# Kernel tuning notes

Hardware: AMD Instinct MI355X
Metric: run time of the kernel (lower is better)

The kernel has to match this reference:

```python
import jax, jax.numpy as jnp
import numpy as np

N_HEADS = 16
D_EMB = 1024
D_HEAD = D_EMB // N_HEADS


def setup_inputs() -> dict:
    key = jax.random.key(0)
    ks = jax.random.split(key, 5)
    scale = 1.0 / np.sqrt(D_EMB)
    x = jax.random.normal(ks[0], (4, 2048, D_EMB), dtype=jnp.float32)
    W_in = jax.random.normal(ks[1], (3 * D_EMB, D_EMB), dtype=jnp.float32) * scale
    b_in = jax.random.normal(ks[2], (3 * D_EMB,), dtype=jnp.float32) * 0.01
    W_out = jax.random.normal(ks[3], (D_EMB, D_EMB), dtype=jnp.float32) * scale
    b_out = jax.random.normal(ks[4], (D_EMB,), dtype=jnp.float32) * 0.01
    return {"x": x, "W_in": W_in, "b_in": b_in, "W_out": W_out, "b_out": b_out}


def reference(x, W_in, b_in, W_out, b_out):
    b, s, d = x.shape
    qkv = x @ W_in.T + b_in  # [b, s, 3d]
    q, k, v = jnp.split(qkv, 3, axis=-1)
    def heads(t):
        return t.reshape(b, s, N_HEADS, D_HEAD).transpose(0, 2, 1, 3)  # [b,h,s,dh]
    q, k, v = heads(q), heads(k), heads(v)
    scores = jnp.einsum('bhqd,bhkd->bhqk', q, k)
    causal = jnp.tril(jnp.ones((s, s), dtype=bool))  # keep lower-triangular incl diag
    scores = jnp.where(causal, scores, -jnp.inf)
    scores = scores / np.sqrt(D_HEAD).astype(np.float32)
    w = jax.nn.softmax(scores, axis=-1)
    out = jnp.einsum('bhqk,bhkd->bhqd', w, v)  # [b,h,s,dh]
    out = out.transpose(0, 2, 1, 3).reshape(b, s, d)
    return out @ W_out.T + b_out
```

## Files before the change

### kernel.cpp

```cpp
#include <hip/hip_runtime.h>
#include <hip/hip_bf16.h>
#include <cstdint>


typedef float  floatx4  __attribute__((ext_vector_type(4)));
typedef __bf16 bf16x8   __attribute__((ext_vector_type(8)));
typedef __bf16 bf16x4   __attribute__((ext_vector_type(4)));
typedef short  shortx4  __attribute__((ext_vector_type(4)));
typedef unsigned int   uint32x2 __attribute__((ext_vector_type(2)));
typedef unsigned short ushortx8 __attribute__((ext_vector_type(8)));

#define MFMA16(a,b,c) __builtin_amdgcn_mfma_f32_16x16x32_bf16(a, b, c, 0, 0, 0)

__device__ __forceinline__ floatx4 mfma_k16(bf16x4 a, bf16x4 b, floatx4 c) {
#if defined(__HIP_DEVICE_COMPILE__)
#if __has_builtin(__builtin_amdgcn_mfma_f32_16x16x16_bf16)
  return __builtin_amdgcn_mfma_f32_16x16x16_bf16(a, b, c, 0, 0, 0);
#elif __has_builtin(__builtin_amdgcn_mfma_f32_16x16x16bf16_1k)
  return __builtin_amdgcn_mfma_f32_16x16x16bf16_1k(
      __builtin_bit_cast(shortx4, a), __builtin_bit_cast(shortx4, b), c, 0, 0, 0);
#else
  floatx4 d;
  asm("v_mfma_f32_16x16x16_bf16 %0, %1, %2, %3"
      : "=v"(d)
      : "v"(__builtin_bit_cast(uint32x2, a)),
        "v"(__builtin_bit_cast(uint32x2, b)), "v"(c));
  return d;
#endif
#else
  (void)a; (void)b;
  return c;
#endif
}

__device__ __forceinline__ float fast_exp2(float x) {
#if defined(__HIP_DEVICE_COMPILE__)
#if __has_builtin(__builtin_amdgcn_exp2f)
  return __builtin_amdgcn_exp2f(x);
#else
  float r;
  asm("v_exp_f32 %0, %1" : "=v"(r) : "v"(x));
  return r;
#endif
#else
  return x;
#endif
}

#define C_SCALE 0.18033688011112042f
#define M_STATIC 16.0f

__device__ __forceinline__ void gload_lds16(const void* g, void* l) {
  __builtin_amdgcn_global_load_lds(
      (__attribute__((address_space(1))) void*)(g),
      (__attribute__((address_space(3))) void*)(l), 16, 0, 0);
}

#define N_X4    2097152
#define N_WIN4  786432
#define N_WOUT4 262144
#define N_B4    768
__global__ __launch_bounds__(256) void cast_fused(
    const float* __restrict__ x, const float* __restrict__ W_in,
    const float* __restrict__ W_out, const float* __restrict__ b_in,
    __bf16* __restrict__ xb, __bf16* __restrict__ Winb,
    __bf16* __restrict__ Woutb, float* __restrict__ bins) {
  int i = blockIdx.x * 256 + threadIdx.x;
  if (i < N_X4) {
    const float4 v = ((const float4*)x)[i];
    bf16x4 o;
    o.x = (__bf16)v.x; o.y = (__bf16)v.y; o.z = (__bf16)v.z; o.w = (__bf16)v.w;
    ((bf16x4*)xb)[i] = o;
  } else if (i < N_X4 + N_WIN4) {
    const int j = i - N_X4;
    const float s = (j < 262144) ? C_SCALE : 1.0f;
    const float4 v = ((const float4*)W_in)[j];
    bf16x4 o;
    o.x = (__bf16)(v.x * s); o.y = (__bf16)(v.y * s);
    o.z = (__bf16)(v.z * s); o.w = (__bf16)(v.w * s);
    ((bf16x4*)Winb)[j] = o;
  } else if (i < N_X4 + N_WIN4 + N_WOUT4) {
    const int j = i - N_X4 - N_WIN4;
    const float4 v = ((const float4*)W_out)[j];
    bf16x4 o;
    o.x = (__bf16)v.x; o.y = (__bf16)v.y; o.z = (__bf16)v.z; o.w = (__bf16)v.w;
    ((bf16x4*)Woutb)[j] = o;
  } else {
    const int j = i - N_X4 - N_WIN4 - N_WOUT4;
    const float s = (j < 256) ? C_SCALE : 1.0f;
    float4 v = ((const float4*)b_in)[j];
    v.x *= s; v.y *= s; v.z *= s; v.w *= s;
    ((float4*)bins)[j] = v;
  }
}

template <int MODE>
__global__ __launch_bounds__(256) void gemm_bt(
    const __bf16* __restrict__ A, const __bf16* __restrict__ B,
    const float* __restrict__ bias, void* __restrict__ Cout,
    __bf16* __restrict__ Vt, int M, int N, int K) {
  __shared__ __bf16 As[128 * 32];
  __shared__ __bf16 Bs[128 * 32];
  const int tid = threadIdx.x;
  const int wave = tid >> 6, lane = tid & 63;
  const int quad = lane >> 4, l15 = lane & 15;
  const int wm = (wave & 1) * 64, wn = (wave >> 1) * 64;
  const long row0 = (long)blockIdx.y * 128;
  const long col0 = (long)blockIdx.x * 128;

  floatx4 acc[4][4] = {};

  const int sr = wave * 16 + (lane >> 2);
  const int sc = (lane & 3) * 8;
  const __bf16* ga = A + (row0 + sr) * (long)K + sc;
  const __bf16* gb = B + (col0 + sr) * (long)K + sc;
  __bf16* lA = As + wave * 512 + lane * 8;
  __bf16* lB = Bs + wave * 512 + lane * 8;

  for (int k0 = 0; k0 < K; k0 += 32) {
    gload_lds16(ga,                lA);
    gload_lds16(ga + 64 * (long)K, lA + 2048);
    gload_lds16(gb,                lB);
    gload_lds16(gb + 64 * (long)K, lB + 2048);
    ga += 32; gb += 32;
    __syncthreads();

    bf16x8 af[4], bfr[4];
#pragma unroll
    for (int i = 0; i < 4; ++i)
      af[i] = *(const bf16x8*)(As + (wm + i * 16 + l15) * 32 + quad * 8);
#pragma unroll
    for (int j = 0; j < 4; ++j)
      bfr[j] = *(const bf16x8*)(Bs + (wn + j * 16 + l15) * 32 + quad * 8);
#pragma unroll
    for (int i = 0; i < 4; ++i)
#pragma unroll
      for (int j = 0; j < 4; ++j)
        acc[i][j] = MFMA16(af[i], bfr[j], acc[i][j]);
    __syncthreads();
  }

#pragma unroll
  for (int i = 0; i < 4; ++i) {
    const long r0 = row0 + wm + i * 16 + quad * 4;
#pragma unroll
    for (int j = 0; j < 4; ++j) {
      const long c = col0 + wn + j * 16 + l15;
      const float bv = bias[c];
      if (MODE == 0) {
#pragma unroll
        for (int reg = 0; reg < 4; ++reg)
          ((float*)Cout)[(r0 + reg) * (long)N + c] = acc[i][j][reg] + bv;
      } else {
        if (c < 2048) {
#pragma unroll
          for (int reg = 0; reg < 4; ++reg)
            ((__bf16*)Cout)[(r0 + reg) * (long)N + c] =
                (__bf16)(acc[i][j][reg] + bv);
        } else {
          const int cc = (int)c - 2048;
          const int hh = cc >> 6, dh = cc & 63;
          const int bb = (int)(r0 >> 11), s = (int)(r0 & 2047);
          bf16x4 pk;
#pragma unroll
          for (int reg = 0; reg < 4; ++reg)
            pk[reg] = (__bf16)(acc[i][j][reg] + bv);
          *(bf16x4*)(Vt + ((long)(bb * 16 + hh) * 64 + dh) * 2048 + s) = pk;
        }
      }
    }
  }
}

__global__ __launch_bounds__(256, 4) void flash_attn(
    const __bf16* __restrict__ qkv,
    const __bf16* __restrict__ Vt,
    __bf16* __restrict__ Out) {
  constexpr int S = 2048;
  const int h = blockIdx.y, b = blockIdx.z;
  const int x = (int)(blockIdx.x + 5 * blockIdx.z + 3 * blockIdx.y) & 15;
  const int qtA = x, qtB = 31 - x;
  const int kmaxA = qtA + 1;
  const int kmax  = qtB + 1;

  __shared__ __bf16 Ks[2][64 * 72];
  __shared__ __bf16 Vs[2][64 * 72];

  const int tid = threadIdx.x, wave = tid >> 6, lane = tid & 63;
  const int quad = lane >> 4, l15 = lane & 15;

  bf16x8 qf[2][2];
  {
    const long qrA = (long)(b * S + qtA * 64 + wave * 16 + l15) * 3072 + h * 64;
    const long qrB = (long)(b * S + qtB * 64 + wave * 16 + l15) * 3072 + h * 64;
    qf[0][0] = *(const bf16x8*)(qkv + qrA + quad * 8);
    qf[0][1] = *(const bf16x8*)(qkv + qrA + 32 + quad * 8);
    qf[1][0] = *(const bf16x8*)(qkv + qrB + quad * 8);
    qf[1][1] = *(const bf16x8*)(qkv + qrB + 32 + quad * 8);
  }

  bf16x4 ones4;
#pragma unroll
  for (int j = 0; j < 4; ++j) ones4[j] = (__bf16)1.0f;

  floatx4 oA[4] = {}, oB[4] = {};
  floatx4 lA = {0.f, 0.f, 0.f, 0.f}, lB = {0.f, 0.f, 0.f, 0.f};

  const int srow = tid >> 3;
  const int sc8 = (tid & 7) * 8;
  const __bf16* ka = qkv + ((long)(b * S) + srow) * 3072 + 1024 + h * 64 + sc8;
  const __bf16* va = Vt + ((long)(b * 16 + h) * 64 + srow) * S + sc8;
  const int sl = srow * 72 + sc8;

  ushortx8 kr0 = *(const ushortx8*)ka;
  ushortx8 kr1 = *(const ushortx8*)(ka + 32 * 3072);
  ushortx8 vr0 = *(const ushortx8*)va;
  ushortx8 vr1 = *(const ushortx8*)(va + 32 * (long)S);
  *(ushortx8*)(&Ks[0][sl]) = kr0;
  *(ushortx8*)(&Ks[0][sl + 32 * 72]) = kr1;
  *(ushortx8*)(&Vs[0][sl]) = vr0;
  *(ushortx8*)(&Vs[0][sl + 32 * 72]) = vr1;
  kr0 = *(const ushortx8*)(ka + 64 * 3072);
  kr1 = *(const ushortx8*)(ka + 96 * 3072);
  vr0 = *(const ushortx8*)(va + 64);
  vr1 = *(const ushortx8*)(va + 32 * (long)S + 64);
  const __bf16* kn = ka + 128 * 3072;
  const __bf16* vn = va + 128;
  __syncthreads();

  for (int kt = 0; kt < kmax; ++kt) {
    const int cur = kt & 1;
    if (kt + 1 < kmax) {
      *(ushortx8*)(&Ks[cur ^ 1][sl]) = kr0;
      *(ushortx8*)(&Ks[cur ^ 1][sl + 32 * 72]) = kr1;
      *(ushortx8*)(&Vs[cur ^ 1][sl]) = vr0;
      *(ushortx8*)(&Vs[cur ^ 1][sl + 32 * 72]) = vr1;
    }
    if (kt + 2 < kmax) {
      kr0 = *(const ushortx8*)kn;
      kr1 = *(const ushortx8*)(kn + 32 * 3072);
      vr0 = *(const ushortx8*)vn;
      vr1 = *(const ushortx8*)(vn + 32 * (long)S);
      kn += 64 * 3072; vn += 64;
    }

    const bool actA = (kt < kmaxA);
    const bool partA = (kt == qtA);
    const bool partB = (kt == qtB);

    floatx4 svA[4], svB[4];
    __builtin_amdgcn_s_setprio(1);
#pragma unroll
    for (int nb = 0; nb < 4; ++nb) {
      const bf16x8 k0 = *(const bf16x8*)(&Ks[cur][(nb * 16 + l15) * 72 + quad * 8]);
      const bf16x8 k1 = *(const bf16x8*)(&Ks[cur][(nb * 16 + l15) * 72 + 32 + quad * 8]);
      if (actA) {
        floatx4 z = {0.f, 0.f, 0.f, 0.f};
        z = MFMA16(k0, qf[0][0], z);
        z = MFMA16(k1, qf[0][1], z);
        svA[nb] = z;
      }
      {
        floatx4 z = {0.f, 0.f, 0.f, 0.f};
        z = MFMA16(k0, qf[1][0], z);
        z = MFMA16(k1, qf[1][1], z);
        svB[nb] = z;
      }
    }
    __builtin_amdgcn_s_setprio(0);

    if (partA) {
      const int qg = qtA * 64 + wave * 16 + l15;
#pragma unroll
      for (int nb = 0; nb < 4; ++nb) {
        const int key0 = kt * 64 + nb * 16 + quad * 4;
#pragma unroll
        for (int r = 0; r < 4; ++r)
          if (key0 + r > qg) svA[nb][r] = -1.0e30f;
      }
    }
    if (partB) {
      const int qg = qtB * 64 + wave * 16 + l15;
#pragma unroll
      for (int nb = 0; nb < 4; ++nb) {
        const int key0 = kt * 64 + nb * 16 + quad * 4;
#pragma unroll
        for (int r = 0; r < 4; ++r)
          if (key0 + r > qg) svB[nb][r] = -1.0e30f;
      }
    }

    bf16x4 pfA[4], pfB[4];
    if (actA) {
#pragma unroll
      for (int nb = 0; nb < 4; ++nb)
#pragma unroll
        for (int r = 0; r < 4; ++r)
          pfA[nb][r] = (__bf16)fast_exp2(svA[nb][r] - M_STATIC);
#pragma unroll
      for (int c = 0; c < 4; ++c) lA = mfma_k16(ones4, pfA[c], lA);
    }
    {
#pragma unroll
      for (int nb = 0; nb < 4; ++nb)
#pragma unroll
        for (int r = 0; r < 4; ++r)
          pfB[nb][r] = (__bf16)fast_exp2(svB[nb][r] - M_STATIC);
#pragma unroll
      for (int c = 0; c < 4; ++c) lB = mfma_k16(ones4, pfB[c], lB);
    }

    __builtin_amdgcn_s_setprio(1);
#pragma unroll
    for (int mb = 0; mb < 4; ++mb) {
#pragma unroll
      for (int c = 0; c < 4; ++c) {
        const bf16x4 vf = *(const bf16x4*)(&Vs[cur][(mb * 16 + l15) * 72 + c * 16 + quad * 4]);
        if (actA) oA[mb] = mfma_k16(vf, pfA[c], oA[mb]);
        oB[mb] = mfma_k16(vf, pfB[c], oB[mb]);
      }
    }
    __builtin_amdgcn_s_setprio(0);
    __syncthreads();
  }

  {
    const float inv = 1.f / lA[0];
    const long row = (long)(b * S + qtA * 64 + wave * 16 + l15);
#pragma unroll
    for (int mb = 0; mb < 4; ++mb) {
      bf16x4 pk;
#pragma unroll
      for (int r = 0; r < 4; ++r) pk[r] = (__bf16)(oA[mb][r] * inv);
      *(bf16x4*)(Out + row * 1024 + h * 64 + mb * 16 + quad * 4) = pk;
    }
  }
  {
    const float inv = 1.f / lB[0];
    const long row = (long)(b * S + qtB * 64 + wave * 16 + l15);
#pragma unroll
    for (int mb = 0; mb < 4; ++mb) {
      bf16x4 pk;
#pragma unroll
      for (int r = 0; r < 4; ++r) pk[r] = (__bf16)(oB[mb][r] * inv);
      *(bf16x4*)(Out + row * 1024 + h * 64 + mb * 16 + quad * 4) = pk;
    }
  }
}

extern "C" void kernel_launch(void* const* d_in, const int* in_sizes, int n_in,
                              void* d_out, int out_size, void* d_ws, size_t ws_size,
                              hipStream_t stream) {
  const float* x     = (const float*)d_in[0];
  const float* W_in  = (const float*)d_in[1];
  const float* b_in  = (const float*)d_in[2];
  const float* W_out = (const float*)d_in[3];
  const float* b_out = (const float*)d_in[4];

  const int BS = 4 * 2048;
  const int D = 1024, N3 = 3072;

  char* w = (char*)d_ws;
  __bf16* xb    = (__bf16*)w;  w += (size_t)BS * D * 2;
  __bf16* Winb  = (__bf16*)w;  w += (size_t)N3 * D * 2;
  __bf16* Woutb = (__bf16*)w;  w += (size_t)D * D * 2;
  __bf16* qkvb  = (__bf16*)w;  w += (size_t)BS * N3 * 2;
  __bf16* Vtb   = (__bf16*)w;  w += (size_t)64 * 64 * 2048 * 2;
  __bf16* attnb = (__bf16*)w;  w += (size_t)BS * D * 2;
  float*  bins  = (float*)w;   w += (size_t)N3 * 4;

  const int castN = N_X4 + N_WIN4 + N_WOUT4 + N_B4;
  cast_fused<<<dim3(castN / 256), 256, 0, stream>>>(
      x, W_in, W_out, b_in, xb, Winb, Woutb, bins);

  gemm_bt<2><<<dim3(N3 / 128, BS / 128), 256, 0, stream>>>(
      xb, Winb, bins, (void*)qkvb, Vtb, BS, N3, D);

  flash_attn<<<dim3(16, 16, 4), 256, 0, stream>>>(qkvb, Vtb, attnb);

  gemm_bt<0><<<dim3(D / 128, BS / 128), 256, 0, stream>>>(
      attnb, Woutb, b_out, d_out, nullptr, BS, D, D);
}
```

Measured before the change: 268.5 us.

## Deepen GEMM K-tile to 64 with XOR-swizzled LDS and remapped workgroup order

The bf16 GEMM kernel now stages a K depth of 64 per iteration instead of 32, which halves the number of barrier pairs and load rounds per tile. LDS rows are XOR-swizzled on 16-byte chunks so the wider 128-byte rows do not cause bank conflicts on fragment reads. Workgroup IDs are also remapped with a stride-8 permutation, presumably to spread neighbouring tiles across XCDs or improve L2 locality. LDS use doubles to 32 KB per block, which may lower occupancy, and the remap assumes the grid size is divisible by 8.

Measured after the change: 249.9 us. 1.07x faster.

```diff
diff --git a/kernel.cpp b/kernel.cpp
--- a/kernel.cpp
+++ b/kernel.cpp
@@ -99,44 +99,56 @@
     const __bf16* __restrict__ A, const __bf16* __restrict__ B,
     const float* __restrict__ bias, void* __restrict__ Cout,
     __bf16* __restrict__ Vt, int M, int N, int K) {
-  __shared__ __bf16 As[128 * 32];
-  __shared__ __bf16 Bs[128 * 32];
+  __shared__ __bf16 As[128 * 64];
+  __shared__ __bf16 Bs[128 * 64];
   const int tid = threadIdx.x;
   const int wave = tid >> 6, lane = tid & 63;
   const int quad = lane >> 4, l15 = lane & 15;
   const int wm = (wave & 1) * 64, wn = (wave >> 1) * 64;
-  const long row0 = (long)blockIdx.y * 128;
-  const long col0 = (long)blockIdx.x * 128;
+
+  const int nwg = (int)(gridDim.x * gridDim.y);
+  int f = (int)(blockIdx.y * gridDim.x + blockIdx.x);
+  f = (f & 7) * (nwg >> 3) + (f >> 3);
+  const int bx = f % (int)gridDim.x;
+  const int by = f / (int)gridDim.x;
+  const long row0 = (long)by * 128;
+  const long col0 = (long)bx * 128;
 
   floatx4 acc[4][4] = {};
 
-  const int sr = wave * 16 + (lane >> 2);
-  const int sc = (lane & 3) * 8;
-  const __bf16* ga = A + (row0 + sr) * (long)K + sc;
-  const __bf16* gb = B + (col0 + sr) * (long)K + sc;
-  __bf16* lA = As + wave * 512 + lane * 8;
-  __bf16* lB = Bs + wave * 512 + lane * 8;
-
-  for (int k0 = 0; k0 < K; k0 += 32) {
-    gload_lds16(ga,                lA);
-    gload_lds16(ga + 64 * (long)K, lA + 2048);
-    gload_lds16(gb,                lB);
-    gload_lds16(gb + 64 * (long)K, lB + 2048);
-    ga += 32; gb += 32;
+  const int sr = tid >> 3;
+  const int swz = 8 * ((tid & 7) ^ (sr & 7));
+  const __bf16* ga = A + (row0 + sr) * (long)K + swz;
+  const __bf16* gb = B + (col0 + sr) * (long)K + swz;
+  __bf16* lA = As + tid * 8;
+  __bf16* lB = Bs + tid * 8;
+  const int rswz = (l15 & 7) * 8;
+
+  for (int k0 = 0; k0 < K; k0 += 64) {
+#pragma unroll
+    for (int c = 0; c < 4; ++c) {
+      gload_lds16(ga + (long)(32 * c) * K, lA + c * 2048);
+      gload_lds16(gb + (long)(32 * c) * K, lB + c * 2048);
+    }
+    ga += 64; gb += 64;
     __syncthreads();
 
-    bf16x8 af[4], bfr[4];
-#pragma unroll
-    for (int i = 0; i < 4; ++i)
-      af[i] = *(const bf16x8*)(As + (wm + i * 16 + l15) * 32 + quad * 8);
-#pragma unroll
-    for (int j = 0; j < 4; ++j)
-      bfr[j] = *(const bf16x8*)(Bs + (wn + j * 16 + l15) * 32 + quad * 8);
-#pragma unroll
-    for (int i = 0; i < 4; ++i)
+#pragma unroll
+    for (int kh = 0; kh < 2; ++kh) {
+      const int kc = (kh * 32 + quad * 8) ^ rswz;
+      bf16x8 af[4], bfr[4];
+#pragma unroll
+      for (int i = 0; i < 4; ++i)
+        af[i] = *(const bf16x8*)(As + (wm + i * 16 + l15) * 64 + kc);
 #pragma unroll
       for (int j = 0; j < 4; ++j)
-        acc[i][j] = MFMA16(af[i], bfr[j], acc[i][j]);
+        bfr[j] = *(const bf16x8*)(Bs + (wn + j * 16 + l15) * 64 + kc);
+#pragma unroll
+      for (int i = 0; i < 4; ++i)
+#pragma unroll
+        for (int j = 0; j < 4; ++j)
+          acc[i][j] = MFMA16(af[i], bfr[j], acc[i][j]);
+    }
     __syncthreads();
   }
 
```
